# Optimization experiments

Hardware: AMD Instinct MI355X
Metric: run time of the kernel (lower is better)

The kernel has to match this reference:

```python
import jax, jax.numpy as jnp
import numpy as np


def _conv1x1(x, w, b):
    # x: [B,C,H,W], w: [O,C], b: [O] -> [B,O,H,W]
    return jnp.einsum('oc,bchw->bohw', w, x) + b[None, :, None, None]


def setup_inputs() -> dict:
    key = jax.random.key(0)
    ks = jax.random.split(key, 9)
    B, C, O, H, W = 8, 192, 96, 64, 64
    s_in = 1.0 / np.sqrt(C)
    s_out = 1.0 / np.sqrt(O)
    return {
        'x': jax.random.normal(ks[0], (B, C, H, W), dtype=jnp.float32),
        'g_w': jax.random.normal(ks[1], (O, C), dtype=jnp.float32) * s_in,
        'g_b': jax.random.normal(ks[2], (O,), dtype=jnp.float32) * s_in,
        'theta_w': jax.random.normal(ks[3], (O, C), dtype=jnp.float32) * s_in,
        'theta_b': jax.random.normal(ks[4], (O,), dtype=jnp.float32) * s_in,
        'phi_w': jax.random.normal(ks[5], (O, C), dtype=jnp.float32) * s_in,
        'phi_b': jax.random.normal(ks[6], (O,), dtype=jnp.float32) * s_in,
        'W_w': jax.random.normal(ks[7], (C, O), dtype=jnp.float32) * s_out,
        'W_b': jax.random.normal(ks[8], (C,), dtype=jnp.float32) * s_out,
    }


def reference(x, g_w, g_b, theta_w, theta_b, phi_w, phi_b, W_w, W_b):
    B, C, H, W = x.shape
    O = g_w.shape[0]
    N = H * W
    # 1x1 conv projections, flattened to [B, O, N]
    g_x = _conv1x1(x, g_w, g_b).reshape(B, O, N)          # [B,O,N]
    theta_x = _conv1x1(x, theta_w, theta_b).reshape(B, O, N)
    phi_x = _conv1x1(x, phi_w, phi_b).reshape(B, O, N)
    # scores f1[b,n,m] = theta[:, :, n] . phi[:, :, m]
    f1 = jnp.einsum('bon,bom->bnm', theta_x, phi_x)       # [B,N,N]
    f_div_C = jax.nn.softmax(f1, axis=-1)
    # y[b,n,o] = sum_m f[b,n,m] * g[b,o,m]
    y = jnp.einsum('bnm,bom->bon', f_div_C, g_x)          # [B,O,N]
    y = y.reshape(B, O, H, W)
    W_y = _conv1x1(y, W_w, W_b)                           # [B,C,H,W]
    return W_y + x
```

## Files before the change

### kernel.cpp

```cpp
#include <hip/hip_runtime.h>

typedef unsigned short u16;
typedef unsigned int u32;
typedef float f32x4 __attribute__((ext_vector_type(4)));
typedef float f32x16 __attribute__((ext_vector_type(16)));
typedef _Float16 h16x8 __attribute__((ext_vector_type(8)));
typedef u32 u32x4 __attribute__((ext_vector_type(4)));
typedef u32 u32x2 __attribute__((ext_vector_type(2)));
typedef u16 u16x4 __attribute__((ext_vector_type(4)));

#define NB 8
#define CC 192
#define OO 96
#define NN 4096
#define NSPLIT 3
#define XPAD 200
#define LOG2E 1.4426950408889634f

static __device__ __forceinline__ u16 f2h(float f) {
  _Float16 h = (_Float16)f;
  return __builtin_bit_cast(u16, h);
}
static __device__ __forceinline__ void gl_lds16(const u16* g, u16* l) {
  __builtin_amdgcn_global_load_lds(
      (const __attribute__((address_space(1))) void*)g,
      (__attribute__((address_space(3))) void*)l, 16, 0, 0);
}
static __device__ __forceinline__ void plane_swap(u32& a, u32& b) {
  u32x2 r = __builtin_amdgcn_permlane32_swap(a, b, false, false);
  a = r[0]; b = r[1];
}
static __device__ __forceinline__ float half_combine_max(float x) {
  u32 a = __builtin_bit_cast(u32, x), b = a;
  plane_swap(a, b);
  return fmaxf(__builtin_bit_cast(float, a), __builtin_bit_cast(float, b));
}
static __device__ __forceinline__ float half_combine_sum(float x) {
  u32 a = __builtin_bit_cast(u32, x), b = a;
  plane_swap(a, b);
  return __builtin_bit_cast(float, a) + __builtin_bit_cast(float, b);
}
static __device__ __forceinline__ float max3f(float a, float b, float c) {
  return fmaxf(fmaxf(a, b), c);
}

__global__ __launch_bounds__(256) void proj_kernel(
    const float* __restrict__ x,
    const float* __restrict__ g_w, const float* __restrict__ g_b,
    const float* __restrict__ th_w, const float* __restrict__ th_b,
    const float* __restrict__ ph_w, const float* __restrict__ ph_b,
    u16* __restrict__ QB, u16* __restrict__ KA, u16* __restrict__ VA)
{
  __shared__ __align__(16) u16 Xs[64][XPAD];
  __shared__ __align__(16) u16 Ws[96][XPAD];
  const int b = blockIdx.y, n0 = blockIdx.x * 64, tid = threadIdx.x;
  const int lane = tid & 63, wv = tid >> 6, l15 = lane & 15, lg = lane >> 4;

  #pragma unroll
  for (int it = 0; it < 12; ++it) {
    int idx = tid + it * 256;
    int c = idx >> 4, q = idx & 15;
    float4 v = *(const float4*)(x + ((size_t)(b * CC + c)) * NN + n0 + q * 4);
    Xs[q * 4 + 0][c] = f2h(v.x); Xs[q * 4 + 1][c] = f2h(v.y);
    Xs[q * 4 + 2][c] = f2h(v.z); Xs[q * 4 + 3][c] = f2h(v.w);
  }

  for (int p = 0; p < 3; ++p) {
    const float* w    = (p == 0) ? th_w : (p == 1) ? ph_w : g_w;
    const float* bias = (p == 0) ? th_b : (p == 1) ? ph_b : g_b;
    const float scale = (p == 0) ? LOG2E : 1.0f;
    __syncthreads();
    #pragma unroll
    for (int it = 0; it < 18; ++it) {
      int idx = tid + it * 256;
      int r = idx / 48, q = idx % 48;
      float4 v = *(const float4*)(w + r * CC + q * 4);
      u16x4 hh; hh[0] = f2h(v.x * scale); hh[1] = f2h(v.y * scale);
      hh[2] = f2h(v.z * scale); hh[3] = f2h(v.w * scale);
      *(u16x4*)&Ws[r][q * 4] = hh;
    }
    __syncthreads();

    f32x4 acc[6];
    #pragma unroll
    for (int of = 0; of < 6; ++of) acc[of] = (f32x4){0.f, 0.f, 0.f, 0.f};
    #pragma unroll
    for (int ks = 0; ks < 6; ++ks) {
      h16x8 xa = *(const h16x8*)&Xs[wv * 16 + l15][ks * 32 + lg * 8];
      #pragma unroll
      for (int of = 0; of < 6; ++of) {
        h16x8 wf = *(const h16x8*)&Ws[of * 16 + l15][ks * 32 + lg * 8];
        if (p < 2) acc[of] = __builtin_amdgcn_mfma_f32_16x16x32_f16(xa, wf, acc[of], 0, 0, 0);
        else       acc[of] = __builtin_amdgcn_mfma_f32_16x16x32_f16(wf, xa, acc[of], 0, 0, 0);
      }
    }

    if (p < 2) {
      u16* dst = (p == 0) ? QB : KA;
      #pragma unroll
      for (int of = 0; of < 6; ++of) {
        int o = of * 16 + l15;
        float bo = bias[o] * scale;
        int kch = of * 2 + (l15 >> 3);
        #pragma unroll
        for (int r = 0; r < 4; ++r) {
          int n = n0 + wv * 16 + lg * 4 + r;
          int idx = (b * 128 + (n >> 5)) * 3072 + (kch * 32 + (n & 31)) * 8 + (o & 7);
          dst[idx] = f2h(acc[of][r] + bo);
        }
      }
    } else {
      #pragma unroll
      for (int of = 0; of < 6; ++of) {
        #pragma unroll
        for (int r = 0; r < 4; ++r) {
          int o = of * 16 + lg * 4 + r;
          int m = n0 + wv * 16 + l15;
          int idx = (b * 256 + (m >> 4)) * 1536 +
                    (((o >> 5) * 2 + ((m >> 3) & 1)) * 32 + (o & 31)) * 8 + (m & 7);
          VA[idx] = f2h(acc[of][r] + bias[o]);
        }
      }
    }
  }
}

__global__ __launch_bounds__(256, 3) void attn_kernel(
    const u16* __restrict__ QB, const u16* __restrict__ KA,
    const u16* __restrict__ VA, u16* __restrict__ yP, float* __restrict__ ml)
{
  __shared__ __align__(16) u16 Ks[2][6144];
  __shared__ __align__(16) u16 Vs[2][6144];
  const int b   = blockIdx.x;
  const int qt  = blockIdx.y;
  const int sp  = blockIdx.z;
  const int tid = threadIdx.x;
  const int lane = tid & 63;
  const int wv  = tid >> 6;
  const int l31 = lane & 31;
  const int h   = lane >> 5;

  const int t_start = (64 * sp) / NSPLIT;
  const int t_end   = (64 * (sp + 1)) / NSPLIT;
  const int nt = t_end - t_start;

  const int nc = qt * 4 + wv;
  const u16* qb = QB + (size_t)(b * 128 + nc) * 3072;
  h16x8 qf[6];
  #pragma unroll
  for (int ks = 0; ks < 6; ++ks)
    qf[ks] = *(const h16x8*)(qb + ((ks * 2 + h) * 32 + l31) * 8);

  const u16* KAb = KA + (size_t)b * (128 * 3072);
  const u16* VAb = VA + (size_t)b * (256 * 1536);

  f32x16 acc[3];
  #pragma unroll
  for (int ob = 0; ob < 3; ++ob)
    #pragma unroll
    for (int i = 0; i < 16; ++i) acc[ob][i] = 0.f;
  float m_run = -3.0e38f, l_run = 0.f;

  {
    const u16* gk = KAb + (size_t)t_start * 6144;
    const u16* gv = VAb + (size_t)t_start * 6144;
    #pragma unroll
    for (int i = 0; i < 3; ++i) gl_lds16(gk + tid * 8 + i * 2048, &Ks[0][tid * 8 + i * 2048]);
    #pragma unroll
    for (int i = 0; i < 3; ++i) gl_lds16(gv + tid * 8 + i * 2048, &Vs[0][tid * 8 + i * 2048]);
  }

  for (int t = 0; t < nt; ++t) {
    const int bf = t & 1;
    if (t + 1 < nt) {
      const u16* gk = KAb + (size_t)(t_start + t + 1) * 6144;
      const u16* gv = VAb + (size_t)(t_start + t + 1) * 6144;
      #pragma unroll
      for (int i = 0; i < 3; ++i) gl_lds16(gk + tid * 8 + i * 2048, &Ks[bf ^ 1][tid * 8 + i * 2048]);
      #pragma unroll
      for (int i = 0; i < 3; ++i) gl_lds16(gv + tid * 8 + i * 2048, &Vs[bf ^ 1][tid * 8 + i * 2048]);
      asm volatile("s_waitcnt vmcnt(6)" ::: "memory");
    } else {
      asm volatile("s_waitcnt vmcnt(0)" ::: "memory");
    }
    __builtin_amdgcn_s_barrier();
    __builtin_amdgcn_sched_barrier(0);

    f32x16 S0, S1;
    #pragma unroll
    for (int i = 0; i < 16; ++i) { S0[i] = 0.f; S1[i] = 0.f; }
    const u16* kb0 = &Ks[bf][0];
    const u16* kb1 = &Ks[bf][3072];
    __builtin_amdgcn_s_setprio(1);
    #pragma unroll
    for (int ks = 0; ks < 6; ++ks) {
      h16x8 kf0 = *(const h16x8*)(kb0 + ((ks * 2 + h) * 32 + l31) * 8);
      S0 = __builtin_amdgcn_mfma_f32_32x32x16_f16(kf0, qf[ks], S0, 0, 0, 0);
      h16x8 kf1 = *(const h16x8*)(kb1 + ((ks * 2 + h) * 32 + l31) * 8);
      S1 = __builtin_amdgcn_mfma_f32_32x32x16_f16(kf1, qf[ks], S1, 0, 0, 0);
    }
    __builtin_amdgcn_s_setprio(0);

    float v[16];
    #pragma unroll
    for (int i = 0; i < 16; ++i) v[i] = fmaxf(S0[i], S1[i]);
    float t0 = max3f(v[0], v[1], v[2]),  t1 = max3f(v[3], v[4], v[5]);
    float t2 = max3f(v[6], v[7], v[8]),  t3 = max3f(v[9], v[10], v[11]);
    float t4 = max3f(v[12], v[13], v[14]);
    float pmax = half_combine_max(fmaxf(max3f(t0, t1, t2), max3f(t3, t4, v[15])));
    if (__ballot(pmax > m_run + 11.5416f)) {
      float mn = fmaxf(m_run, pmax);
      float sc = exp2f(m_run - mn);
      m_run = mn; l_run *= sc;
      #pragma unroll
      for (int ob = 0; ob < 3; ++ob)
        #pragma unroll
        for (int i = 0; i < 16; ++i) acc[ob][i] *= sc;
    }
    float p0[16], p1[16];
    #pragma unroll
    for (int i = 0; i < 16; ++i) { p0[i] = exp2f(S0[i] - m_run); p1[i] = exp2f(S1[i] - m_run); }
    #pragma unroll
    for (int i = 0; i < 16; ++i) v[i] = p0[i] + p1[i];
    #pragma unroll
    for (int st = 8; st >= 1; st >>= 1)
      #pragma unroll
      for (int i = 0; i < 8; ++i) if (i < st) v[i] += v[i + st];
    l_run += half_combine_sum(v[0]);

    u32 pk0[8], pk1[8];
    #pragma unroll
    for (int i = 0; i < 8; ++i) {
      pk0[i] = __builtin_bit_cast(u32, __builtin_amdgcn_cvt_pkrtz(p0[2 * i], p0[2 * i + 1]));
      pk1[i] = __builtin_bit_cast(u32, __builtin_amdgcn_cvt_pkrtz(p1[2 * i], p1[2 * i + 1]));
    }
    plane_swap(pk0[0], pk0[2]); plane_swap(pk0[1], pk0[3]);
    plane_swap(pk0[4], pk0[6]); plane_swap(pk0[5], pk0[7]);
    plane_swap(pk1[0], pk1[2]); plane_swap(pk1[1], pk1[3]);
    plane_swap(pk1[4], pk1[6]); plane_swap(pk1[5], pk1[7]);
    u32x4 c00 = {pk0[0], pk0[1], pk0[2], pk0[3]}, c01 = {pk0[4], pk0[5], pk0[6], pk0[7]};
    u32x4 c10 = {pk1[0], pk1[1], pk1[2], pk1[3]}, c11 = {pk1[4], pk1[5], pk1[6], pk1[7]};
    h16x8 pf[4] = {__builtin_bit_cast(h16x8, c00), __builtin_bit_cast(h16x8, c01),
                   __builtin_bit_cast(h16x8, c10), __builtin_bit_cast(h16x8, c11)};

    const u16* vb0 = &Vs[bf][0];
    const u16* vb1 = &Vs[bf][3072];
    __builtin_amdgcn_s_setprio(1);
    #pragma unroll
    for (int s2 = 0; s2 < 2; ++s2) {
      #pragma unroll
      for (int ob = 0; ob < 3; ++ob) {
        h16x8 vf0 = *(const h16x8*)(vb0 + (((s2 * 3 + ob) * 2 + h) * 32 + l31) * 8);
        acc[ob] = __builtin_amdgcn_mfma_f32_32x32x16_f16(vf0, pf[s2], acc[ob], 0, 0, 0);
        h16x8 vf1 = *(const h16x8*)(vb1 + (((s2 * 3 + ob) * 2 + h) * 32 + l31) * 8);
        acc[ob] = __builtin_amdgcn_mfma_f32_32x32x16_f16(vf1, pf[2 + s2], acc[ob], 0, 0, 0);
      }
    }
    __builtin_amdgcn_s_setprio(0);
    __builtin_amdgcn_s_barrier();
    __builtin_amdgcn_sched_barrier(0);
  }

  float inv = 1.0f / l_run;
  int nglob = nc * 32 + l31;
  u16* yp = yP + (((size_t)sp * NB + b) * NN + nglob) * OO;
  #pragma unroll
  for (int ob = 0; ob < 3; ++ob) {
    #pragma unroll
    for (int rq = 0; rq < 4; ++rq) {
      int o0 = ob * 32 + rq * 8 + h * 4;
      u32 w0 = __builtin_bit_cast(u32,
          __builtin_amdgcn_cvt_pkrtz(acc[ob][rq * 4 + 0] * inv, acc[ob][rq * 4 + 1] * inv));
      u32 w1 = __builtin_bit_cast(u32,
          __builtin_amdgcn_cvt_pkrtz(acc[ob][rq * 4 + 2] * inv, acc[ob][rq * 4 + 3] * inv));
      uint2 pr; pr.x = w0; pr.y = w1;
      *(uint2*)&yp[o0] = pr;
    }
  }
  if (h == 0) {
    float2 v2; v2.x = m_run; v2.y = l_run;
    *(float2*)&ml[(((size_t)sp * NB + b) * NN + nglob) * 2] = v2;
  }
}

#define YPAD 104
__global__ __launch_bounds__(256) void outproj_kernel(
    const float* __restrict__ x, const float* __restrict__ Ww,
    const float* __restrict__ Wb, const u16* __restrict__ yP,
    const float* __restrict__ ml, float* __restrict__ out)
{
  __shared__ __align__(16) u16 Wws[CC][YPAD];
  __shared__ __align__(16) u16 Ys[64][YPAD];
  const int b = blockIdx.y, n0 = blockIdx.x * 64, tid = threadIdx.x;
  const int lane = tid & 63, wv = tid >> 6, l15 = lane & 15, lg = lane >> 4;
  const size_t SB = (size_t)NB * NN;

  #pragma unroll
  for (int it = 0; it < 18; ++it) {
    int idx = tid + it * 256;
    int r = idx / 24, q = idx % 24;
    float4 v = *(const float4*)(Ww + r * OO + q * 4);
    u16x4 hh; hh[0] = f2h(v.x); hh[1] = f2h(v.y); hh[2] = f2h(v.z); hh[3] = f2h(v.w);
    *(u16x4*)&Wws[r][q * 4] = hh;
  }
  #pragma unroll
  for (int it = 0; it < 3; ++it) {
    int idx = tid + it * 256;
    int n = idx / 12, q = idx % 12;
    size_t bn = (size_t)b * NN + n0 + n;
    float m0 = ml[(0 * SB + bn) * 2], l0 = ml[(0 * SB + bn) * 2 + 1];
    float m1 = ml[(1 * SB + bn) * 2], l1 = ml[(1 * SB + bn) * 2 + 1];
    float m2 = ml[(2 * SB + bn) * 2], l2 = ml[(2 * SB + bn) * 2 + 1];
    float M = max3f(m0, m1, m2);
    float w0 = l0 * exp2f(m0 - M), w1 = l1 * exp2f(m1 - M), w2 = l2 * exp2f(m2 - M);
    float rinv = 1.0f / (w0 + w1 + w2);
    w0 *= rinv; w1 *= rinv; w2 *= rinv;
    h16x8 y0 = *(const h16x8*)(yP + (0 * SB + bn) * OO + q * 8);
    h16x8 y1 = *(const h16x8*)(yP + (1 * SB + bn) * OO + q * 8);
    h16x8 y2 = *(const h16x8*)(yP + (2 * SB + bn) * OO + q * 8);
    u32x4 packed;
    #pragma unroll
    for (int e = 0; e < 4; ++e) {
      float a = w0 * (float)y0[2 * e]     + w1 * (float)y1[2 * e]     + w2 * (float)y2[2 * e];
      float c = w0 * (float)y0[2 * e + 1] + w1 * (float)y1[2 * e + 1] + w2 * (float)y2[2 * e + 1];
      packed[e] = __builtin_bit_cast(u32, __builtin_amdgcn_cvt_pkrtz(a, c));
    }
    *(u32x4*)&Ys[n][q * 8] = packed;
  }
  __syncthreads();

  f32x4 acc[12];
  #pragma unroll
  for (int cf = 0; cf < 12; ++cf) acc[cf] = (f32x4){0.f, 0.f, 0.f, 0.f};
  #pragma unroll
  for (int ks = 0; ks < 3; ++ks) {
    h16x8 yb = *(const h16x8*)&Ys[wv * 16 + l15][ks * 32 + lg * 8];
    #pragma unroll
    for (int cf = 0; cf < 12; ++cf) {
      h16x8 wa = *(const h16x8*)&Wws[cf * 16 + l15][ks * 32 + lg * 8];
      acc[cf] = __builtin_amdgcn_mfma_f32_16x16x32_f16(wa, yb, acc[cf], 0, 0, 0);
    }
  }
  #pragma unroll
  for (int cf = 0; cf < 12; ++cf) {
    #pragma unroll
    for (int r = 0; r < 4; ++r) {
      int c = cf * 16 + lg * 4 + r;
      size_t off = ((size_t)(b * CC + c)) * NN + n0 + wv * 16 + l15;
      out[off] = acc[cf][r] + x[off] + Wb[c];
    }
  }
}

extern "C" void kernel_launch(void* const* d_in, const int* in_sizes, int n_in,
                              void* d_out, int out_size, void* d_ws, size_t ws_size,
                              hipStream_t stream) {
  const float* x    = (const float*)d_in[0];
  const float* g_w  = (const float*)d_in[1];
  const float* g_b  = (const float*)d_in[2];
  const float* th_w = (const float*)d_in[3];
  const float* th_b = (const float*)d_in[4];
  const float* ph_w = (const float*)d_in[5];
  const float* ph_b = (const float*)d_in[6];
  const float* W_w  = (const float*)d_in[7];
  const float* W_b  = (const float*)d_in[8];
  float* out = (float*)d_out;

  char* ws = (char*)d_ws;
  const size_t projB = (size_t)NB * NN * OO * sizeof(u16);
  u16* QB   = (u16*)ws;
  u16* KA   = (u16*)(ws + projB);
  u16* VA   = (u16*)(ws + 2 * projB);
  u16* yP   = (u16*)(ws + 3 * projB);
  float* ml = (float*)(ws + 6 * projB);

  dim3 blk(256);
  dim3 gproj(64, NB);
  hipLaunchKernelGGL(proj_kernel, gproj, blk, 0, stream,
                     x, g_w, g_b, th_w, th_b, ph_w, ph_b, QB, KA, VA);
  dim3 gattn(NB, 32, NSPLIT);
  hipLaunchKernelGGL(attn_kernel, gattn, blk, 0, stream, QB, KA, VA, yP, ml);
  dim3 gout(64, NB);
  hipLaunchKernelGGL(outproj_kernel, gout, blk, 0, stream, x, W_w, W_b, yP, ml, out);
}
```

Measured before the change: 110.6 us.

## Read K/V fragments directly from global memory instead of LDS double-buffering

Removes the shared-memory double buffer and the global_load_lds staging in the attention kernel, so each wave loads its K and V MFMA fragments straight from global memory (through cache) and processes each 32-key half-tile with its own online-softmax update. This drops the block barriers and LDS traffic. In exchange, the four waves of a block each fetch the same K/V data, so global/L2 traffic goes up and loads are no longer prefetched ahead of use. The softmax max/rescale step now runs twice per 64-key tile. Launch bounds drop from 3 to 2 blocks per SIMD target.

```diff
diff --git a/kernel.cpp b/kernel.cpp
--- a/kernel.cpp
+++ b/kernel.cpp
@@ -20,11 +20,6 @@
 static __device__ __forceinline__ u16 f2h(float f) {
   _Float16 h = (_Float16)f;
   return __builtin_bit_cast(u16, h);
-}
-static __device__ __forceinline__ void gl_lds16(const u16* g, u16* l) {
-  __builtin_amdgcn_global_load_lds(
-      (const __attribute__((address_space(1))) void*)g,
-      (__attribute__((address_space(3))) void*)l, 16, 0, 0);
 }
 static __device__ __forceinline__ void plane_swap(u32& a, u32& b) {
   u32x2 r = __builtin_amdgcn_permlane32_swap(a, b, false, false);
@@ -125,12 +120,10 @@
   }
 }
 
-__global__ __launch_bounds__(256, 3) void attn_kernel(
+__global__ __launch_bounds__(256, 2) void attn_kernel(
     const u16* __restrict__ QB, const u16* __restrict__ KA,
     const u16* __restrict__ VA, u16* __restrict__ yP, float* __restrict__ ml)
 {
-  __shared__ __align__(16) u16 Ks[2][6144];
-  __shared__ __align__(16) u16 Vs[2][6144];
   const int b   = blockIdx.x;
   const int qt  = blockIdx.y;
   const int sp  = blockIdx.z;
@@ -142,7 +135,6 @@
 
   const int t_start = (64 * sp) / NSPLIT;
   const int t_end   = (64 * (sp + 1)) / NSPLIT;
-  const int nt = t_end - t_start;
 
   const int nc = qt * 4 + wv;
   const u16* qb = QB + (size_t)(b * 128 + nc) * 3072;
@@ -161,104 +153,64 @@
     for (int i = 0; i < 16; ++i) acc[ob][i] = 0.f;
   float m_run = -3.0e38f, l_run = 0.f;
 
-  {
-    const u16* gk = KAb + (size_t)t_start * 6144;
-    const u16* gv = VAb + (size_t)t_start * 6144;
-    #pragma unroll
-    for (int i = 0; i < 3; ++i) gl_lds16(gk + tid * 8 + i * 2048, &Ks[0][tid * 8 + i * 2048]);
-    #pragma unroll
-    for (int i = 0; i < 3; ++i) gl_lds16(gv + tid * 8 + i * 2048, &Vs[0][tid * 8 + i * 2048]);
-  }
-
-  for (int t = 0; t < nt; ++t) {
-    const int bf = t & 1;
-    if (t + 1 < nt) {
-      const u16* gk = KAb + (size_t)(t_start + t + 1) * 6144;
-      const u16* gv = VAb + (size_t)(t_start + t + 1) * 6144;
-      #pragma unroll
-      for (int i = 0; i < 3; ++i) gl_lds16(gk + tid * 8 + i * 2048, &Ks[bf ^ 1][tid * 8 + i * 2048]);
-      #pragma unroll
-      for (int i = 0; i < 3; ++i) gl_lds16(gv + tid * 8 + i * 2048, &Vs[bf ^ 1][tid * 8 + i * 2048]);
-      asm volatile("s_waitcnt vmcnt(6)" ::: "memory");
-    } else {
-      asm volatile("s_waitcnt vmcnt(0)" ::: "memory");
-    }
-    __builtin_amdgcn_s_barrier();
-    __builtin_amdgcn_sched_barrier(0);
-
-    f32x16 S0, S1;
-    #pragma unroll
-    for (int i = 0; i < 16; ++i) { S0[i] = 0.f; S1[i] = 0.f; }
-    const u16* kb0 = &Ks[bf][0];
-    const u16* kb1 = &Ks[bf][3072];
-    __builtin_amdgcn_s_setprio(1);
-    #pragma unroll
-    for (int ks = 0; ks < 6; ++ks) {
-      h16x8 kf0 = *(const h16x8*)(kb0 + ((ks * 2 + h) * 32 + l31) * 8);
-      S0 = __builtin_amdgcn_mfma_f32_32x32x16_f16(kf0, qf[ks], S0, 0, 0, 0);
-      h16x8 kf1 = *(const h16x8*)(kb1 + ((ks * 2 + h) * 32 + l31) * 8);
-      S1 = __builtin_amdgcn_mfma_f32_32x32x16_f16(kf1, qf[ks], S1, 0, 0, 0);
-    }
-    __builtin_amdgcn_s_setprio(0);
-
-    float v[16];
-    #pragma unroll
-    for (int i = 0; i < 16; ++i) v[i] = fmaxf(S0[i], S1[i]);
-    float t0 = max3f(v[0], v[1], v[2]),  t1 = max3f(v[3], v[4], v[5]);
-    float t2 = max3f(v[6], v[7], v[8]),  t3 = max3f(v[9], v[10], v[11]);
-    float t4 = max3f(v[12], v[13], v[14]);
-    float pmax = half_combine_max(fmaxf(max3f(t0, t1, t2), max3f(t3, t4, v[15])));
-    if (__ballot(pmax > m_run + 11.5416f)) {
-      float mn = fmaxf(m_run, pmax);
-      float sc = exp2f(m_run - mn);
-      m_run = mn; l_run *= sc;
-      #pragma unroll
-      for (int ob = 0; ob < 3; ++ob)
-        #pragma unroll
-        for (int i = 0; i < 16; ++i) acc[ob][i] *= sc;
-    }
-    float p0[16], p1[16];
-    #pragma unroll
-    for (int i = 0; i < 16; ++i) { p0[i] = exp2f(S0[i] - m_run); p1[i] = exp2f(S1[i] - m_run); }
-    #pragma unroll
-    for (int i = 0; i < 16; ++i) v[i] = p0[i] + p1[i];
-    #pragma unroll
-    for (int st = 8; st >= 1; st >>= 1)
-      #pragma unroll
-      for (int i = 0; i < 8; ++i) if (i < st) v[i] += v[i + st];
-    l_run += half_combine_sum(v[0]);
-
-    u32 pk0[8], pk1[8];
-    #pragma unroll
-    for (int i = 0; i < 8; ++i) {
-      pk0[i] = __builtin_bit_cast(u32, __builtin_amdgcn_cvt_pkrtz(p0[2 * i], p0[2 * i + 1]));
-      pk1[i] = __builtin_bit_cast(u32, __builtin_amdgcn_cvt_pkrtz(p1[2 * i], p1[2 * i + 1]));
-    }
-    plane_swap(pk0[0], pk0[2]); plane_swap(pk0[1], pk0[3]);
-    plane_swap(pk0[4], pk0[6]); plane_swap(pk0[5], pk0[7]);
-    plane_swap(pk1[0], pk1[2]); plane_swap(pk1[1], pk1[3]);
-    plane_swap(pk1[4], pk1[6]); plane_swap(pk1[5], pk1[7]);
-    u32x4 c00 = {pk0[0], pk0[1], pk0[2], pk0[3]}, c01 = {pk0[4], pk0[5], pk0[6], pk0[7]};
-    u32x4 c10 = {pk1[0], pk1[1], pk1[2], pk1[3]}, c11 = {pk1[4], pk1[5], pk1[6], pk1[7]};
-    h16x8 pf[4] = {__builtin_bit_cast(h16x8, c00), __builtin_bit_cast(h16x8, c01),
-                   __builtin_bit_cast(h16x8, c10), __builtin_bit_cast(h16x8, c11)};
-
-    const u16* vb0 = &Vs[bf][0];
-    const u16* vb1 = &Vs[bf][3072];
-    __builtin_amdgcn_s_setprio(1);
-    #pragma unroll
-    for (int s2 = 0; s2 < 2; ++s2) {
-      #pragma unroll
-      for (int ob = 0; ob < 3; ++ob) {
-        h16x8 vf0 = *(const h16x8*)(vb0 + (((s2 * 3 + ob) * 2 + h) * 32 + l31) * 8);
-        acc[ob] = __builtin_amdgcn_mfma_f32_32x32x16_f16(vf0, pf[s2], acc[ob], 0, 0, 0);
-        h16x8 vf1 = *(const h16x8*)(vb1 + (((s2 * 3 + ob) * 2 + h) * 32 + l31) * 8);
-        acc[ob] = __builtin_amdgcn_mfma_f32_32x32x16_f16(vf1, pf[2 + s2], acc[ob], 0, 0, 0);
-      }
-    }
-    __builtin_amdgcn_s_setprio(0);
-    __builtin_amdgcn_s_barrier();
-    __builtin_amdgcn_sched_barrier(0);
+  for (int t = t_start; t < t_end; ++t) {
+    const u16* kt = KAb + (size_t)t * 6144;
+    const u16* vt = VAb + (size_t)t * 6144;
+    #pragma unroll
+    for (int c = 0; c < 2; ++c) {
+      const u16* kc = kt + c * 3072;
+      const u16* vc = vt + c * 3072;
+      f32x16 S;
+      #pragma unroll
+      for (int i = 0; i < 16; ++i) S[i] = 0.f;
+      #pragma unroll
+      for (int ks = 0; ks < 6; ++ks) {
+        h16x8 kf = *(const h16x8*)(kc + ((ks * 2 + h) * 32 + l31) * 8);
+        S = __builtin_amdgcn_mfma_f32_32x32x16_f16(kf, qf[ks], S, 0, 0, 0);
+      }
+      float t0 = max3f(S[0], S[1], S[2]),   t1 = max3f(S[3], S[4], S[5]);
+      float t2 = max3f(S[6], S[7], S[8]),   t3 = max3f(S[9], S[10], S[11]);
+      float t4 = max3f(S[12], S[13], S[14]);
+      float pmax = half_combine_max(fmaxf(max3f(t0, t1, t2), max3f(t3, t4, S[15])));
+      if (__ballot(pmax > m_run + 11.5416f)) {
+        float mn = fmaxf(m_run, pmax);
+        float sc = exp2f(m_run - mn);
+        m_run = mn; l_run *= sc;
+        #pragma unroll
+        for (int ob = 0; ob < 3; ++ob)
+          #pragma unroll
+          for (int i = 0; i < 16; ++i) acc[ob][i] *= sc;
+      }
+      float p[16], v[16];
+      #pragma unroll
+      for (int i = 0; i < 16; ++i) p[i] = exp2f(S[i] - m_run);
+      #pragma unroll
+      for (int i = 0; i < 16; ++i) v[i] = p[i];
+      #pragma unroll
+      for (int st = 8; st >= 1; st >>= 1)
+        #pragma unroll
+        for (int i = 0; i < 8; ++i) if (i < st) v[i] += v[i + st];
+      l_run += half_combine_sum(v[0]);
+      u32 pk[8];
+      #pragma unroll
+      for (int i = 0; i < 8; ++i)
+        pk[i] = __builtin_bit_cast(u32, __builtin_amdgcn_cvt_pkrtz(p[2 * i], p[2 * i + 1]));
+      plane_swap(pk[0], pk[2]); plane_swap(pk[1], pk[3]);
+      plane_swap(pk[4], pk[6]); plane_swap(pk[5], pk[7]);
+      u32x4 bw0 = {pk[0], pk[1], pk[2], pk[3]};
+      u32x4 bw1 = {pk[4], pk[5], pk[6], pk[7]};
+      h16x8 pf0 = __builtin_bit_cast(h16x8, bw0);
+      h16x8 pf1 = __builtin_bit_cast(h16x8, bw1);
+      #pragma unroll
+      for (int s2 = 0; s2 < 2; ++s2) {
+        h16x8 pfr = s2 ? pf1 : pf0;
+        #pragma unroll
+        for (int ob = 0; ob < 3; ++ob) {
+          h16x8 vf = *(const h16x8*)(vc + (((s2 * 3 + ob) * 2 + h) * 32 + l31) * 8);
+          acc[ob] = __builtin_amdgcn_mfma_f32_32x32x16_f16(vf, pfr, acc[ob], 0, 0, 0);
+        }
+      }
+    }
   }
 
   float inv = 1.0f / l_run;
```

Measured after the change: 128.7 us. +16.4%, slower.
